# Kernel optimization log

Hardware: AMD Instinct MI355X
Metric: run time of the kernel (lower is better)

Reference implementation:

```python
import jax, jax.numpy as jnp
import numpy as np

N = 100000   # num_nodes
E = 1600000  # num_edges
R = 8        # num_rels
B = 4        # num_bases
D = 64       # inp_dim = h_dim = out_dim


def setup_inputs() -> dict:
    key = jax.random.key(0)
    ks = jax.random.split(key, 16)
    s = 1.0 / np.sqrt(D)
    inp = {
        'h': jax.random.normal(ks[0], (N, D), jnp.float32),
        'src': jax.random.randint(ks[1], (E,), 0, N),
        'dst': jax.random.randint(ks[2], (E,), 0, N),
        'etype': jax.random.randint(ks[3], (E,), 0, R),
        'norm': jax.random.uniform(ks[4], (E, 1), jnp.float32),
    }
    for i in range(3):  # i2h, hidden, h2o layers (basis decomposition)
        inp[f'bases{i}'] = jax.random.normal(ks[5 + 2 * i], (B, D, D), jnp.float32) * s
        inp[f'wcomp{i}'] = jax.random.normal(ks[6 + 2 * i], (R, B), jnp.float32) * s
    inp['dec_w1'] = jax.random.normal(ks[11], (D, D), jnp.float32) * s
    inp['dec_b1'] = jnp.zeros((D,), jnp.float32)
    inp['dec_w2'] = jax.random.normal(ks[12], (D, 1), jnp.float32) * s
    inp['dec_b2'] = jnp.zeros((1,), jnp.float32)
    return inp


def rgcn_layer(h, src, dst, etype, norm, bases, wcomp, activate):
    # basis decomposition: W_r = sum_b wcomp[r,b] * bases[b]
    W = jnp.einsum('rb,bio->rio', wcomp, bases)           # [R, D, D]
    # transform all nodes under every relation (dense GEMM), then gather per edge
    Ht = jnp.einsum('ni,rio->rno', h, W).reshape(R * N, -1)  # [R*N, D]
    msg = Ht[etype * N + src] * norm                      # [E, D] gather + norm
    out = jax.ops.segment_sum(msg, dst, num_segments=N)   # scatter-add to dst
    return jax.nn.relu(out) if activate else out


def reference(h, src, dst, etype, norm, bases0, wcomp0, bases1, wcomp1,
              bases2, wcomp2, dec_w1, dec_b1, dec_w2, dec_b2):
    # EncoderRGCN: i2h (relu) -> hidden (relu) -> h2o (no activation)
    h1 = rgcn_layer(h, src, dst, etype, norm, bases0, wcomp0, True)
    h2 = rgcn_layer(h1, src, dst, etype, norm, bases1, wcomp1, True)
    henc = rgcn_layer(h2, src, dst, etype, norm, bases2, wcomp2, False)
    # AttributeDecoder: Linear -> ReLU -> Linear(reconstruct_dim=1)
    d1 = jax.nn.relu(henc @ dec_w1 + dec_b1)
    rec = (d1 @ dec_w2 + dec_b2).squeeze()                # [N]
    return rec, henc
```

## Files before the change

### kernel.cpp

```cpp
#include <hip/hip_runtime.h>

typedef _Float16 half8 __attribute__((ext_vector_type(8)));
typedef _Float16 half4 __attribute__((ext_vector_type(4)));
typedef _Float16 half2v __attribute__((ext_vector_type(2)));
typedef float floatx4 __attribute__((ext_vector_type(4)));

constexpr int NN = 100000;
constexpr int EE = 1600000;
constexpr int NBK = 391;
constexpr int CHUNK = 3125;
constexpr int CAPB = 6144;
constexpr int LCAP = 4608;
constexpr int NDCAP = 48;

__global__ __launch_bounds__(512) void k_partprep(const int* __restrict__ dst,
                                                  const int* __restrict__ src,
                                                  const int* __restrict__ etype,
                                                  const float* __restrict__ norm,
                                                  int* __restrict__ gcur,
                                                  int2* __restrict__ part,
                                                  const float* __restrict__ h,
                                                  _Float16* __restrict__ hh,
                                                  const float* __restrict__ b0,
                                                  const float* __restrict__ b1,
                                                  const float* __restrict__ b2,
                                                  _Float16* __restrict__ bbt) {
  __shared__ int2 ldata[CHUNK];
  __shared__ unsigned short lbkt[CHUNK];
  __shared__ int lhist[NBK], lbase[NBK + 1], lcur[NBK], gbase[NBK];
  __shared__ int swsum[8];
  const int tid = threadIdx.x;
  const int bx = blockIdx.x;

  if (bx >= 512) {
    if (bx < 3637) {
      const int i = (bx - 512) * 512 + tid;
      const float4 v = *(const float4*)&h[(size_t)i * 4];
      half4 o = {(_Float16)v.x, (_Float16)v.y, (_Float16)v.z, (_Float16)v.w};
      *(half4*)&hh[(size_t)i * 4] = o;
    } else {
      const int L = (bx - 3637) * 512 + tid;
      const int g = L >> 14;
      const int idx = L & 16383;
      const float* bases = (g == 0) ? b0 : (g == 1) ? b1 : b2;
      const int o = idx >> 8, k = idx & 255;
      const int b = k >> 6, i = k & 63;
      bbt[g * 16384 + idx] = (_Float16)bases[b * 4096 + i * 64 + o];
    }
    return;
  }

  const int e0 = bx * CHUNK;

  if (tid < NBK) lhist[tid] = 0;
  __syncthreads();
  for (int i = tid; i < CHUNK; i += 512)
    atomicAdd(&lhist[dst[e0 + i] >> 8], 1);
  __syncthreads();
  {
    const int v = (tid < NBK) ? lhist[tid] : 0;
    int incl = v;
    for (int d = 1; d < 64; d <<= 1) {
      const int t = __shfl_up(incl, d);
      if ((tid & 63) >= d) incl += t;
    }
    if ((tid & 63) == 63) swsum[tid >> 6] = incl;
    __syncthreads();
    int pre = 0;
    for (int w = 0; w < (tid >> 6); ++w) pre += swsum[w];
    const int excl = pre + incl - v;
    if (tid < NBK) {
      lbase[tid] = excl;
      lcur[tid] = 0;
      gbase[tid] = tid * CAPB + atomicAdd(&gcur[tid], v);
    }
    if (tid == 0) lbase[NBK] = CHUNK;
  }
  __syncthreads();
  for (int i = tid; i < CHUNK; i += 512) {
    const int e = e0 + i;
    const int d = dst[e], s = src[e], et = etype[e];
    const _Float16 nh = (_Float16)norm[e];
    const unsigned short n16 = __builtin_bit_cast(unsigned short, nh);
    const int bk = d >> 8;
    const int pos = lbase[bk] + atomicAdd(&lcur[bk], 1);
    ldata[pos] = make_int2((d << 15) | (s >> 2), (s & 3) | (et << 2) | ((int)n16 << 5));
    lbkt[pos] = (unsigned short)bk;
  }
  __syncthreads();
  for (int i = tid; i < CHUNK; i += 512) {
    const int bk = (int)lbkt[i];
    part[gbase[bk] + (i - lbase[bk])] = ldata[i];
  }
}

__global__ __launch_bounds__(1024) void k_part2(const int* __restrict__ gcur,
                                                const int2* __restrict__ part,
                                                int* __restrict__ off,
                                                int2* __restrict__ em) {
  __shared__ int2 lrec[LCAP];
  __shared__ int hcnt[256];
  __shared__ int wred[16];
  __shared__ int swsum[4];
  const int tid = threadIdx.x;
  const int bk = blockIdx.x;
  const int nb0 = bk << 8;
  const int2* __restrict__ pp = part + (size_t)bk * CAPB;

  {
    int pv = (tid < bk) ? gcur[tid] : 0;
    for (int d = 32; d > 0; d >>= 1) pv += __shfl_down(pv, d);
    if ((tid & 63) == 0) wred[tid >> 6] = pv;
  }
  if (tid < 256) hcnt[tid] = 0;
  __syncthreads();
  int base = 0;
#pragma unroll
  for (int w = 0; w < 16; ++w) base += wred[w];
  const int cntb = gcur[bk];
  const bool uselds = (cntb <= LCAP);

  if (uselds) {
    for (int i = tid; i < cntb; i += 1024) {
      const int2 r = pp[i];
      lrec[i] = r;
      atomicAdd(&hcnt[(((unsigned)r.x) >> 15) & 255], 1);
    }
  } else {
    for (int i = tid; i < cntb; i += 1024)
      atomicAdd(&hcnt[(((unsigned)pp[i].x) >> 15) & 255], 1);
  }
  __syncthreads();
  const int v = (tid < 256) ? hcnt[tid] : 0;
  int incl = v;
  for (int d = 1; d < 64; d <<= 1) {
    const int t = __shfl_up(incl, d);
    if ((tid & 63) >= d) incl += t;
  }
  if (tid < 256 && (tid & 63) == 63) swsum[tid >> 6] = incl;
  __syncthreads();
  if (tid < 256) {
    int pre = 0;
    for (int w = 0; w < (tid >> 6); ++w) pre += swsum[w];
    const int excl = pre + incl - v;
    const int n = nb0 + tid;
    if (n < NN) off[n] = base + excl;
    hcnt[tid] = excl;
  }
  if (bk == NBK - 1 && tid == 0) off[NN] = EE;
  __syncthreads();
  for (int i = tid; i < cntb; i += 1024) {
    const int2 r = uselds ? lrec[i] : pp[i];
    const int d = ((unsigned)r.x) >> 15;
    const int s = ((r.x & 0x7FFF) << 2) | (r.y & 3);
    const int et = (r.y >> 2) & 7;
    const unsigned short n16 = (unsigned short)((r.y >> 5) & 0xFFFF);
    const float nf = (float)__builtin_bit_cast(_Float16, n16);
    const int pos = atomicAdd(&hcnt[d & 255], 1);
    em[base + pos] = make_int2(((d & 15) << 23) | (et << 20) | s, __float_as_int(nf));
  }
}

__global__ __launch_bounds__(256, 8) void k_layer(const _Float16* __restrict__ hh,
                                                  const int* __restrict__ off,
                                                  const int2* __restrict__ em,
                                                  const float* __restrict__ wcomp,
                                                  const _Float16* __restrict__ bbt,
                                                  _Float16* __restrict__ out16,
                                                  float* __restrict__ out32) {
  __shared__ _Float16 Ash[16 * 264];
  __shared__ int  ems_s[16 * NDCAP];
  __shared__ int2 ems_c[16 * NDCAP];
  __shared__ float4 wcs[8];
  __shared__ int offs[17];
  __shared__ int ovf;
  const int tid = threadIdx.x;
  const int lane = tid & 63;
  const int wv = tid >> 6;
  const int n0 = blockIdx.x * 16;

  if (tid < 17) offs[tid] = off[n0 + tid];
  if (tid == 0) ovf = 0;
  if (tid < 8) wcs[tid] = ((const float4*)wcomp)[tid];
  {
    const int4 z4 = make_int4(0, 0, 0, 0);
    int4* zs = (int4*)ems_s;
    int4* zc = (int4*)ems_c;
    if (tid < 192) zs[tid] = z4;
    for (int i = tid; i < 384; i += 256) zc[i] = z4;
  }
  __syncthreads();

  const int e0 = offs[0];
  const int len = offs[16] - e0;
  for (int i = tid; i < len; i += 256) {
    const int g = e0 + i;
    const int2 r = em[g];
    const int lo = (r.x >> 23) & 15;
    const int rank = g - offs[lo];
    const int et = (r.x >> 20) & 7;
    const int s = r.x & 0xFFFFF;
    const float nf = __int_as_float(r.y);
    const float4 w = wcs[et];
    const int p01i = __builtin_bit_cast(int, __builtin_amdgcn_cvt_pkrtz(nf * w.x, nf * w.y));
    const int p23i = __builtin_bit_cast(int, __builtin_amdgcn_cvt_pkrtz(nf * w.z, nf * w.w));
    if (rank < NDCAP) {
      ems_s[lo * NDCAP + rank] = s;
      ems_c[lo * NDCAP + rank] = make_int2(p01i, p23i);
    } else ovf = 1;
  }
  __syncthreads();

#define LOADB(mm, bb, hv)                                                      \
  {                                                                            \
    const int4* sp4_ = (const int4*)&ems_s[(mm) * NDCAP + (bb) * 16 + eg * 8]; \
    const int4 sa_ = sp4_[0], sb_ = sp4_[1];                                   \
    hv[0] = hp[(unsigned)sa_.x * 32u + fl];                                    \
    hv[1] = hp[(unsigned)sa_.y * 32u + fl];                                    \
    hv[2] = hp[(unsigned)sa_.z * 32u + fl];                                    \
    hv[3] = hp[(unsigned)sa_.w * 32u + fl];                                    \
    hv[4] = hp[(unsigned)sb_.x * 32u + fl];                                    \
    hv[5] = hp[(unsigned)sb_.y * 32u + fl];                                    \
    hv[6] = hp[(unsigned)sb_.z * 32u + fl];                                    \
    hv[7] = hp[(unsigned)sb_.w * 32u + fl];                                    \
  }

#define FMAQ(mm, bb, hv, aq)                                                   \
  {                                                                            \
    const int4* cp4_ = (const int4*)&ems_c[(mm) * NDCAP + (bb) * 16 + eg * 8]; \
    _Pragma("unroll")                                                          \
    for (int k_ = 0; k_ < 4; ++k_) {                                           \
      const int4 c_ = cp4_[k_];                                                \
      const half2v pa01_ = __builtin_bit_cast(half2v, c_.x);                   \
      const half2v pa23_ = __builtin_bit_cast(half2v, c_.y);                   \
      const half2v pb01_ = __builtin_bit_cast(half2v, c_.z);                   \
      const half2v pb23_ = __builtin_bit_cast(half2v, c_.w);                   \
      aq[0] = aq[0] + hv[2 * k_] * __builtin_shufflevector(pa01_, pa01_, 0, 0);\
      aq[1] = aq[1] + hv[2 * k_] * __builtin_shufflevector(pa01_, pa01_, 1, 1);\
      aq[2] = aq[2] + hv[2 * k_] * __builtin_shufflevector(pa23_, pa23_, 0, 0);\
      aq[3] = aq[3] + hv[2 * k_] * __builtin_shufflevector(pa23_, pa23_, 1, 1);\
      aq[0] = aq[0] + hv[2 * k_ + 1] * __builtin_shufflevector(pb01_, pb01_, 0, 0);\
      aq[1] = aq[1] + hv[2 * k_ + 1] * __builtin_shufflevector(pb01_, pb01_, 1, 1);\
      aq[2] = aq[2] + hv[2 * k_ + 1] * __builtin_shufflevector(pb23_, pb23_, 0, 0);\
      aq[3] = aq[3] + hv[2 * k_ + 1] * __builtin_shufflevector(pb23_, pb23_, 1, 1);\
    }                                                                          \
  }

  if (!ovf) {
    const int fl = lane & 31;
    const int eg = lane >> 5;
    const half2v* __restrict__ hp = (const half2v*)hh;
    const int mb = wv * 4;
    const int oA = offs[mb], oB = offs[mb + 1], oC = offs[mb + 2],
              oD = offs[mb + 3], oE = offs[mb + 4];
    const int c0n = oB - oA, c1n = oC - oB, c2n = oD - oC, c3n = oE - oD;
    const int nb0_ = (c0n > 0) ? ((c0n + 15) >> 4) : 1;
    const int nb1_ = (c1n > 0) ? ((c1n + 15) >> 4) : 1;
    const int nb2_ = (c2n > 0) ? ((c2n + 15) >> 4) : 1;
    const int nb3_ = (c3n > 0) ? ((c3n + 15) >> 4) : 1;

    half2v acc[4][4];
#pragma unroll
    for (int q = 0; q < 4; ++q)
#pragma unroll
      for (int i = 0; i < 4; ++i) acc[q][i] = half2v{0, 0};

    half2v hvA[8], hvB[8];
    LOADB(mb, 0, hvA);
#pragma unroll
    for (int q = 0; q < 4; ++q) {
      const int m = mb + q;
      const int nbq = (q == 0) ? nb0_ : (q == 1) ? nb1_ : (q == 2) ? nb2_ : nb3_;
      if (q < 3) {
        if (q & 1) LOADB(m + 1, 0, hvA) else LOADB(m + 1, 0, hvB)
      }
      if (q & 1) FMAQ(m, 0, hvB, acc[q]) else FMAQ(m, 0, hvA, acc[q])
      for (int b = 1; b < nbq; ++b) {
        if (q & 1) {
          LOADB(m, b, hvB) FMAQ(m, b, hvB, acc[q])
        } else {
          LOADB(m, b, hvA) FMAQ(m, b, hvA, acc[q])
        }
      }
    }
#pragma unroll
    for (int q = 0; q < 4; ++q) {
      const int m = mb + q;
#pragma unroll
      for (int i = 0; i < 4; ++i)
        acc[q][i] = acc[q][i] + __builtin_bit_cast(half2v,
            __shfl_xor(__builtin_bit_cast(int, acc[q][i]), 32));
      if (eg == 0) {
        _Float16* ar = &Ash[m * 264];
        *(half2v*)&ar[0 * 64 + 2 * fl] = acc[q][0];
        *(half2v*)&ar[1 * 64 + 2 * fl] = acc[q][1];
        *(half2v*)&ar[2 * 64 + 2 * fl] = acc[q][2];
        *(half2v*)&ar[3 * 64 + 2 * fl] = acc[q][3];
      }
    }
  } else {
    const _Float16* hl = hh + lane;
    for (int q = 0; q < 4; ++q) {
      const int m = wv * 4 + q;
      const int p0 = offs[m], p1 = offs[m + 1];
      float a0 = 0.f, a1 = 0.f, a2 = 0.f, a3 = 0.f;
      for (int p = p0; p < p1; p += 8) {
#pragma unroll
        for (int j = 0; j < 8; ++j) {
          const bool live = (p + j < p1);
          const int idx = live ? p + j : p1 - 1;
          const int2 mm = em[idx];
          const float hv = (float)hl[(size_t)(mm.x & 0xFFFFF) << 6];
          const float wn = live ? __int_as_float(mm.y) : 0.f;
          const float4 w = wcs[(mm.x >> 20) & 7];
          const float t = wn * hv;
          a0 = fmaf(t, w.x, a0); a1 = fmaf(t, w.y, a1);
          a2 = fmaf(t, w.z, a2); a3 = fmaf(t, w.w, a3);
        }
      }
      _Float16* ar = &Ash[m * 264];
      ar[lane]       = (_Float16)a0;
      ar[64 + lane]  = (_Float16)a1;
      ar[128 + lane] = (_Float16)a2;
      ar[192 + lane] = (_Float16)a3;
    }
  }
  __syncthreads();

  const int col = lane & 15;
  const int quad = lane >> 4;
  const int obase = wv * 16 + col;
  const _Float16* ap = &Ash[col * 264 + quad * 8];
  const _Float16* bp = &bbt[(size_t)obase * 256 + quad * 8];
  floatx4 acc2 = {0.f, 0.f, 0.f, 0.f};
#pragma unroll
  for (int s = 0; s < 8; ++s) {
    const half8 af = *(const half8*)(ap + s * 32);
    const half8 bf = *(const half8*)(bp + s * 32);
    acc2 = __builtin_amdgcn_mfma_f32_16x16x32_f16(af, bf, acc2, 0, 0, 0);
  }
  if (out16) {
#pragma unroll
    for (int r = 0; r < 4; ++r) {
      const float c = fmaxf(acc2[r], 0.f);
      out16[(size_t)(n0 + quad * 4 + r) * 64 + obase] = (_Float16)c;
    }
  } else {
#pragma unroll
    for (int r = 0; r < 4; ++r) {
      out32[(size_t)(n0 + quad * 4 + r) * 64 + obase] = acc2[r];
    }
  }
#undef LOADB
#undef FMAQ
}

__global__ __launch_bounds__(256) void k_dec(const float* __restrict__ henc,
                                             const float* __restrict__ w1,
                                             const float* __restrict__ b1,
                                             const float* __restrict__ w2,
                                             const float* __restrict__ b2,
                                             float* __restrict__ rec) {
  __shared__ float w1s[64 * 64];
  __shared__ float hs[16 * 68];
  const int tid = threadIdx.x;
  for (int r = tid; r < 1024; r += 256)
    *(float4*)&w1s[r * 4] = *(const float4*)&w1[r * 4];
  const int og = tid & 15;
  const int nl = tid >> 4;
  const float4 wv2 = *(const float4*)&w2[og * 4];
  const float4 bv1 = *(const float4*)&b1[og * 4];
  const float b2v = b2[0];
  for (int t0 = blockIdx.x * 16; t0 < NN; t0 += gridDim.x * 16) {
    __syncthreads();
    {
      const float4 hv = *(const float4*)&henc[(size_t)t0 * 64 + tid * 4];
      *(float4*)&hs[(tid >> 4) * 68 + (tid & 15) * 4] = hv;
    }
    __syncthreads();
    float4 acc = bv1;
    const float* hr = &hs[nl * 68];
#pragma unroll 8
    for (int i = 0; i < 64; ++i) {
      const float hv = hr[i];
      const float4 wv = *(const float4*)&w1s[i * 64 + og * 4];
      acc.x = fmaf(hv, wv.x, acc.x); acc.y = fmaf(hv, wv.y, acc.y);
      acc.z = fmaf(hv, wv.z, acc.z); acc.w = fmaf(hv, wv.w, acc.w);
    }
    acc.x = fmaxf(acc.x, 0.f); acc.y = fmaxf(acc.y, 0.f);
    acc.z = fmaxf(acc.z, 0.f); acc.w = fmaxf(acc.w, 0.f);
    float v = acc.x * wv2.x + acc.y * wv2.y + acc.z * wv2.z + acc.w * wv2.w;
    v += __shfl_xor(v, 1); v += __shfl_xor(v, 2);
    v += __shfl_xor(v, 4); v += __shfl_xor(v, 8);
    if (og == 0) rec[t0 + nl] = v + b2v;
  }
}


extern "C" void kernel_launch(void* const* d_in, const int* in_sizes, int n_in,
                              void* d_out, int out_size, void* d_ws, size_t ws_size,
                              hipStream_t stream) {
  const float* h     = (const float*)d_in[0];
  const int*   src   = (const int*)d_in[1];
  const int*   dst   = (const int*)d_in[2];
  const int*   etype = (const int*)d_in[3];
  const float* norm  = (const float*)d_in[4];
  const float* bases[3] = {(const float*)d_in[5], (const float*)d_in[7], (const float*)d_in[9]};
  const float* wcomp[3] = {(const float*)d_in[6], (const float*)d_in[8], (const float*)d_in[10]};
  const float* dw1 = (const float*)d_in[11];
  const float* db1 = (const float*)d_in[12];
  const float* dw2 = (const float*)d_in[13];
  const float* db2 = (const float*)d_in[14];

  float* rec  = (float*)d_out;
  float* henc = (float*)d_out + NN;

  char* ws = (char*)d_ws;
  int*      off    = (int*)(ws + 0);
  int*      gcur   = (int*)(ws + 400512);
  int2*     em     = (int2*)(ws + 402560);
  _Float16* hh     = (_Float16*)(ws + 13202560);
  _Float16* h1f    = (_Float16*)(ws + 26002560);
  _Float16* h2f    = (_Float16*)(ws + 38802560);
  _Float16* bbt    = (_Float16*)(ws + 51602560);
  int2*     part   = (int2*)h1f;

  hipMemsetAsync(gcur, 0, NBK * sizeof(int), stream);

  k_partprep<<<3733, 512, 0, stream>>>(dst, src, etype, norm, gcur, part,
                                       h, hh, bases[0], bases[1], bases[2], bbt);
  k_part2<<<NBK, 1024, 0, stream>>>(gcur, part, off, em);

  k_layer<<<NN / 16, 256, 0, stream>>>(hh,  off, em, wcomp[0], bbt,         h1f, nullptr);
  k_layer<<<NN / 16, 256, 0, stream>>>(h1f, off, em, wcomp[1], bbt + 16384, h2f, nullptr);
  k_layer<<<NN / 16, 256, 0, stream>>>(h2f, off, em, wcomp[2], bbt + 32768, nullptr, henc);

  k_dec<<<1024, 256, 0, stream>>>(henc, dw1, db1, dw2, db2, rec);
}
```

Before: 318.1 us.

## Fuse attribute decoder into final RGCN layer and trim LDS zeroing

The separate decoder kernel is removed. The last layer's fp32 output tile is staged through shared memory, and the Linear-ReLU-Linear decoder runs in the same block, so henc is not re-read from global memory and one launch goes away. The LDS edge-slot zeroing now clears only the padding slots past each node's edge count, not the whole buffers. The decoder now reads dw1 directly from global or cache instead of staging it in LDS, which may add load latency per block.

```diff
diff --git a/kernel.cpp b/kernel.cpp
--- a/kernel.cpp
+++ b/kernel.cpp
@@ -167,7 +167,12 @@
                                                   const float* __restrict__ wcomp,
                                                   const _Float16* __restrict__ bbt,
                                                   _Float16* __restrict__ out16,
-                                                  float* __restrict__ out32) {
+                                                  float* __restrict__ out32,
+                                                  const float* __restrict__ dw1,
+                                                  const float* __restrict__ db1,
+                                                  const float* __restrict__ dw2,
+                                                  const float* __restrict__ db2,
+                                                  float* __restrict__ rec) {
   __shared__ _Float16 Ash[16 * 264];
   __shared__ int  ems_s[16 * NDCAP];
   __shared__ int2 ems_c[16 * NDCAP];
@@ -182,14 +187,18 @@
   if (tid < 17) offs[tid] = off[n0 + tid];
   if (tid == 0) ovf = 0;
   if (tid < 8) wcs[tid] = ((const float4*)wcomp)[tid];
+  __syncthreads();
+
   {
-    const int4 z4 = make_int4(0, 0, 0, 0);
-    int4* zs = (int4*)ems_s;
-    int4* zc = (int4*)ems_c;
-    if (tid < 192) zs[tid] = z4;
-    for (int i = tid; i < 384; i += 256) zc[i] = z4;
-  }
-  __syncthreads();
+    const int n = tid >> 4, j = tid & 15;
+    const int cnt = offs[n + 1] - offs[n];
+    const int nb = (cnt > 0) ? ((cnt + 15) >> 4) : 1;
+    const int sl = cnt + j;
+    if (sl < nb * 16 && sl < NDCAP) {
+      ems_s[n * NDCAP + sl] = 0;
+      ems_c[n * NDCAP + sl] = make_int2(0, 0);
+    }
+  }
 
   const int e0 = offs[0];
   const int len = offs[16] - e0;
@@ -350,50 +359,33 @@
     for (int r = 0; r < 4; ++r) {
       out32[(size_t)(n0 + quad * 4 + r) * 64 + obase] = acc2[r];
     }
-  }
-#undef LOADB
-#undef FMAQ
-}
-
-__global__ __launch_bounds__(256) void k_dec(const float* __restrict__ henc,
-                                             const float* __restrict__ w1,
-                                             const float* __restrict__ b1,
-                                             const float* __restrict__ w2,
-                                             const float* __restrict__ b2,
-                                             float* __restrict__ rec) {
-  __shared__ float w1s[64 * 64];
-  __shared__ float hs[16 * 68];
-  const int tid = threadIdx.x;
-  for (int r = tid; r < 1024; r += 256)
-    *(float4*)&w1s[r * 4] = *(const float4*)&w1[r * 4];
-  const int og = tid & 15;
-  const int nl = tid >> 4;
-  const float4 wv2 = *(const float4*)&w2[og * 4];
-  const float4 bv1 = *(const float4*)&b1[og * 4];
-  const float b2v = b2[0];
-  for (int t0 = blockIdx.x * 16; t0 < NN; t0 += gridDim.x * 16) {
     __syncthreads();
-    {
-      const float4 hv = *(const float4*)&henc[(size_t)t0 * 64 + tid * 4];
-      *(float4*)&hs[(tid >> 4) * 68 + (tid & 15) * 4] = hv;
-    }
+    float* hsd = (float*)Ash;
+#pragma unroll
+    for (int r = 0; r < 4; ++r)
+      hsd[(quad * 4 + r) * 68 + obase] = acc2[r];
     __syncthreads();
-    float4 acc = bv1;
-    const float* hr = &hs[nl * 68];
+    const int og = tid & 15;
+    const int nl = tid >> 4;
+    const float4 wv2 = *(const float4*)&dw2[og * 4];
+    float4 dacc = *(const float4*)&db1[og * 4];
+    const float* hr = &hsd[nl * 68];
 #pragma unroll 8
     for (int i = 0; i < 64; ++i) {
       const float hv = hr[i];
-      const float4 wv = *(const float4*)&w1s[i * 64 + og * 4];
-      acc.x = fmaf(hv, wv.x, acc.x); acc.y = fmaf(hv, wv.y, acc.y);
-      acc.z = fmaf(hv, wv.z, acc.z); acc.w = fmaf(hv, wv.w, acc.w);
-    }
-    acc.x = fmaxf(acc.x, 0.f); acc.y = fmaxf(acc.y, 0.f);
-    acc.z = fmaxf(acc.z, 0.f); acc.w = fmaxf(acc.w, 0.f);
-    float v = acc.x * wv2.x + acc.y * wv2.y + acc.z * wv2.z + acc.w * wv2.w;
-    v += __shfl_xor(v, 1); v += __shfl_xor(v, 2);
-    v += __shfl_xor(v, 4); v += __shfl_xor(v, 8);
-    if (og == 0) rec[t0 + nl] = v + b2v;
-  }
+      const float4 wv = *(const float4*)&dw1[i * 64 + og * 4];
+      dacc.x = fmaf(hv, wv.x, dacc.x); dacc.y = fmaf(hv, wv.y, dacc.y);
+      dacc.z = fmaf(hv, wv.z, dacc.z); dacc.w = fmaf(hv, wv.w, dacc.w);
+    }
+    dacc.x = fmaxf(dacc.x, 0.f); dacc.y = fmaxf(dacc.y, 0.f);
+    dacc.z = fmaxf(dacc.z, 0.f); dacc.w = fmaxf(dacc.w, 0.f);
+    float vdec = dacc.x * wv2.x + dacc.y * wv2.y + dacc.z * wv2.z + dacc.w * wv2.w;
+    vdec += __shfl_xor(vdec, 1); vdec += __shfl_xor(vdec, 2);
+    vdec += __shfl_xor(vdec, 4); vdec += __shfl_xor(vdec, 8);
+    if (og == 0) rec[n0 + nl] = vdec + db2[0];
+  }
+#undef LOADB
+#undef FMAQ
 }
 
 
@@ -431,9 +423,10 @@
                                        h, hh, bases[0], bases[1], bases[2], bbt);
   k_part2<<<NBK, 1024, 0, stream>>>(gcur, part, off, em);
 
-  k_layer<<<NN / 16, 256, 0, stream>>>(hh,  off, em, wcomp[0], bbt,         h1f, nullptr);
-  k_layer<<<NN / 16, 256, 0, stream>>>(h1f, off, em, wcomp[1], bbt + 16384, h2f, nullptr);
-  k_layer<<<NN / 16, 256, 0, stream>>>(h2f, off, em, wcomp[2], bbt + 32768, nullptr, henc);
-
-  k_dec<<<1024, 256, 0, stream>>>(henc, dw1, db1, dw2, db2, rec);
+  k_layer<<<NN / 16, 256, 0, stream>>>(hh,  off, em, wcomp[0], bbt,         h1f, nullptr,
+                                       nullptr, nullptr, nullptr, nullptr, nullptr);
+  k_layer<<<NN / 16, 256, 0, stream>>>(h1f, off, em, wcomp[1], bbt + 16384, h2f, nullptr,
+                                       nullptr, nullptr, nullptr, nullptr, nullptr);
+  k_layer<<<NN / 16, 256, 0, stream>>>(h2f, off, em, wcomp[2], bbt + 32768, nullptr, henc,
+                                       dw1, db1, dw2, db2, rec);
 }
```

New measurement: 337.8 us. 6.2% more time.
